# Kernel tuning notes

Hardware: AMD Instinct MI355X
Metric: run time of the kernel (lower is better)

## Reference

```python
import jax, jax.numpy as jnp
import numpy as np

N = 100000
E = 1600000
IN_C, HID_C, OUT_C = 40, 64, 3


def _sage_params(key, f_in, f_out):
    k1, k2, k3 = jax.random.split(key, 3)
    s = 1.0 / np.sqrt(f_in)
    return (jax.random.uniform(k1, (f_in, f_out), jnp.float32, -s, s),  # W_neigh (lin_l)
            jax.random.uniform(k2, (f_in, f_out), jnp.float32, -s, s),  # W_root  (lin_r)
            jax.random.uniform(k3, (f_out,), jnp.float32, -s, s))       # bias


def setup_inputs() -> dict:
    key = jax.random.key(0)
    ks = jax.random.split(key, 8)
    x = jax.random.normal(ks[0], (N, IN_C), jnp.float32)
    edge_index = jax.random.randint(ks[1], (2, E), 0, N, jnp.int64)
    dims = [(IN_C, HID_C), (HID_C, HID_C), (HID_C, OUT_C),   # encoder
            (OUT_C, HID_C), (HID_C, HID_C), (HID_C, IN_C)]   # decoder
    names = ['enc1', 'enc2', 'enc3', 'dec1', 'dec2', 'dec3']
    out = {'x': x, 'edge_index': edge_index}
    for name, (fi, fo), k in zip(names, dims, ks[2:]):
        Wl, Wr, b = _sage_params(k, fi, fo)
        out[name + '_Wl'] = Wl
        out[name + '_Wr'] = Wr
        out[name + '_b'] = b
    return out


def _sage_conv(h, src, dst, inv_deg, Wl, Wr, b):
    # mean-aggregate neighbor features (messages src -> dst), then linear.
    msg_sum = jax.ops.segment_sum(h[src], dst, num_segments=N)  # [N, F_in]
    agg = msg_sum * inv_deg                                      # mean aggregation
    return agg @ Wl + h @ Wr + b


def reference(x, edge_index,
              enc1_Wl, enc1_Wr, enc1_b, enc2_Wl, enc2_Wr, enc2_b,
              enc3_Wl, enc3_Wr, enc3_b, dec1_Wl, dec1_Wr, dec1_b,
              dec2_Wl, dec2_Wr, dec2_b, dec3_Wl, dec3_Wr, dec3_b):
    src, dst = edge_index[0], edge_index[1]
    deg = jax.ops.segment_sum(jnp.ones((E,), jnp.float32), dst, num_segments=N)
    inv_deg = (1.0 / jnp.maximum(deg, 1.0))[:, None]
    # encoder
    h = jax.nn.relu(_sage_conv(x, src, dst, inv_deg, enc1_Wl, enc1_Wr, enc1_b))
    h = jax.nn.relu(_sage_conv(h, src, dst, inv_deg, enc2_Wl, enc2_Wr, enc2_b))
    z = _sage_conv(h, src, dst, inv_deg, enc3_Wl, enc3_Wr, enc3_b)
    # decoder
    h = jax.nn.relu(_sage_conv(z, src, dst, inv_deg, dec1_Wl, dec1_Wr, dec1_b))
    h = jax.nn.relu(_sage_conv(h, src, dst, inv_deg, dec2_Wl, dec2_Wr, dec2_b))
    x_rec = _sage_conv(h, src, dst, inv_deg, dec3_Wl, dec3_Wr, dec3_b)
    return (x_rec, z)
```

## Files before the change

### kernel.cpp

```cpp
#include <hip/hip_runtime.h>
#include <stdint.h>

#define NNODES 100000
#define NEDGES 1600000
#define NB 98
#define WIN 25000
#define NSL 64
#define SLICE 25000

typedef unsigned short ushort_t;
typedef __attribute__((ext_vector_type(8))) short bf16x8;
typedef __attribute__((ext_vector_type(4))) float f32x4;

__device__ __forceinline__ float b2f(ushort_t u) {
  union { float f; uint32_t i; } v; v.i = ((uint32_t)u) << 16; return v.f;
}
__device__ __forceinline__ float blo(uint32_t p) {
  union { float f; uint32_t i; } v; v.i = p << 16; return v.f;
}
__device__ __forceinline__ float bhi(uint32_t p) {
  union { float f; uint32_t i; } v; v.i = p & 0xffff0000u; return v.f;
}
__device__ __forceinline__ ushort_t f2b(float f) {
  union { float f; uint32_t i; } v; v.f = f;
  uint32_t r = (v.i + 0x7fffu + ((v.i >> 16) & 1u)) >> 16;
  return (ushort_t)r;
}
__device__ __forceinline__ uint32_t pack2(float lo, float hi) {
  return (uint32_t)f2b(lo) | ((uint32_t)f2b(hi) << 16);
}
__device__ __forceinline__ int clampn(int i) {
  return i < 0 ? 0 : (i >= NNODES ? NNODES - 1 : i);
}

__global__ void detect_k(const uint32_t* __restrict__ x, const uint32_t* __restrict__ ei,
                         int* __restrict__ flags) {
  if (blockIdx.x == 0 && threadIdx.x == 0) {
    int cf = 0, ci = 0;
    for (int i = 0; i < 256; ++i) {
      uint32_t u = x[i];
      uint32_t e = (u >> 7) & 0xFFu;
      if (e >= 100u && e <= 141u) cf++;
      if (ei[2 * i + 1] == 0u) ci++;
    }
    flags[0] = (cf >= 128) ? 1 : 0;
    flags[1] = (ci >= 128) ? 1 : 0;
  }
}

__global__ void zero_i32(int* __restrict__ p, int n) {
  int i = blockIdx.x * blockDim.x + threadIdx.x;
  if (i < n) p[i] = 0;
}

__global__ __launch_bounds__(1024) void histw2_k(const uint32_t* __restrict__ ei,
                                                 int* __restrict__ degp,
                                                 const int* __restrict__ flags) {
  __shared__ int h[WIN];
  int b = blockIdx.x;
  int w = b >> 6, s = b & 63;
  for (int j = threadIdx.x; j < WIN; j += 1024) h[j] = 0;
  __syncthreads();
  int i64 = flags[1];
  int base = w * WIN;
  int e0 = s * SLICE, e1 = e0 + SLICE;
  for (int e = e0 + threadIdx.x; e < e1; e += 1024) {
    int d = i64 ? (int)ei[2 * (size_t)NEDGES + 2 * (size_t)e] : (int)ei[(size_t)NEDGES + e];
    d = clampn(d);
    int j = d - base;
    if ((unsigned)j < (unsigned)WIN) atomicAdd(&h[j], 1);
  }
  __syncthreads();
  int* dp = degp + (size_t)s * NNODES + base;
  for (int j = threadIdx.x; j < WIN; j += 1024) dp[j] = h[j];
}

__global__ void hreduce_k(int* __restrict__ degp, int* __restrict__ deg) {
  int n = blockIdx.x * blockDim.x + threadIdx.x;
  if (n >= NNODES) return;
  int run = 0;
  for (int s = 0; s < NSL; ++s) {
    size_t idx = (size_t)s * NNODES + n;
    int t = degp[idx];
    degp[idx] = run;
    run += t;
  }
  deg[n] = run;
}

__global__ __launch_bounds__(1024) void scan1_k(const int* __restrict__ deg, int* __restrict__ bsum) {
  __shared__ int wsum[16];
  int tid = threadIdx.x;
  int i = blockIdx.x * 1024 + tid;
  int v = (i < NNODES) ? deg[i] : 0;
  #pragma unroll
  for (int d = 32; d >= 1; d >>= 1) v += __shfl_down(v, d);
  if ((tid & 63) == 0) wsum[tid >> 6] = v;
  __syncthreads();
  if (tid == 0) {
    int t = 0;
    #pragma unroll
    for (int w = 0; w < 16; ++w) t += wsum[w];
    bsum[blockIdx.x] = t;
  }
}

__global__ void scan2_k(int* __restrict__ bsum, int* __restrict__ offs) {
  if (blockIdx.x == 0 && threadIdx.x == 0) {
    int run = 0;
    for (int b = 0; b < NB; ++b) { int t = bsum[b]; bsum[b] = run; run += t; }
    offs[NNODES] = run;
  }
}

__global__ __launch_bounds__(1024) void scan3_k(const int* __restrict__ deg, const int* __restrict__ bsum,
                                                int* __restrict__ offs, int* __restrict__ cursor,
                                                float* __restrict__ invd) {
  __shared__ int wsum[16];
  int tid = threadIdx.x;
  int lane = tid & 63, wid = tid >> 6;
  int i = blockIdx.x * 1024 + tid;
  int v = (i < NNODES) ? deg[i] : 0;
  int s = v;
  #pragma unroll
  for (int d = 1; d < 64; d <<= 1) {
    int t = __shfl_up(s, d);
    if (lane >= d) s += t;
  }
  if (lane == 63) wsum[wid] = s;
  __syncthreads();
  int wprefix = 0;
  #pragma unroll
  for (int w = 0; w < 16; ++w)
    if (w < wid) wprefix += wsum[w];
  if (i < NNODES) {
    int excl = bsum[blockIdx.x] + wprefix + s - v;
    offs[i] = excl;
    cursor[i] = excl;
    invd[i] = 1.0f / fmaxf((float)v, 1.0f);
  }
}

__global__ void scatter4_k(const uint32_t* __restrict__ ei, int* __restrict__ cursor,
                           int* __restrict__ csr, const int* __restrict__ flags,
                           int lo, int hi) {
  int e = blockIdx.x * blockDim.x + threadIdx.x;
  if (e >= NEDGES) return;
  int i64 = flags[1];
  int s, d;
  if (i64) {
    d = (int)ei[2 * (size_t)NEDGES + 2 * (size_t)e];
    d = clampn(d);
    if (d < lo || d >= hi) return;
    s = (int)ei[2 * (size_t)e];
  } else {
    d = (int)ei[(size_t)NEDGES + e];
    d = clampn(d);
    if (d < lo || d >= hi) return;
    s = (int)ei[e];
  }
  int p = atomicAdd(&cursor[d], 1);
  if (p >= 0 && p < NEDGES) csr[p] = clampn(s);
}

template <bool BF16>
__global__ void cvt_packx_k(const void* __restrict__ src, uint32_t* __restrict__ dst, int npairs,
                            const int* __restrict__ flags) {
  if (flags[0] != (BF16 ? 1 : 0)) return;
  int i = blockIdx.x * blockDim.x + threadIdx.x;
  if (i < npairs) {
    if constexpr (BF16) dst[i] = ((const uint32_t*)src)[i];
    else {
      const float* s = (const float*)src;
      dst[i] = pack2(s[2 * i], s[2 * i + 1]);
    }
  }
}

template <bool BF16>
__global__ void cvt_outp_k(const uint32_t* __restrict__ src, void* __restrict__ dst, int npairs,
                           const int* __restrict__ flags) {
  if (flags[0] != (BF16 ? 1 : 0)) return;
  int i = blockIdx.x * blockDim.x + threadIdx.x;
  if (i < npairs) {
    if constexpr (BF16) ((uint32_t*)dst)[i] = src[i];
    else {
      uint32_t w = src[i];
      float* d = (float*)dst;
      d[2 * i] = blo(w);
      d[2 * i + 1] = bhi(w);
    }
  }
}

template <bool BF16>
__global__ void cvt_out_k(const float* __restrict__ src, void* __restrict__ dst, int n,
                          const int* __restrict__ flags) {
  if (flags[0] != (BF16 ? 1 : 0)) return;
  int i = blockIdx.x * blockDim.x + threadIdx.x;
  if (i < n) {
    if constexpr (BF16) ((ushort_t*)dst)[i] = f2b(src[i]);
    else ((float*)dst)[i] = src[i];
  }
}

struct WPtrs { const void* p[18]; int sz[18]; int off[18]; };

template <bool BF16>
__global__ void cvt_w_k(WPtrs w, float* __restrict__ dst, const int* __restrict__ flags) {
  if (flags[0] != (BF16 ? 1 : 0)) return;
  int a = blockIdx.x;
  int sz = w.sz[a], off = w.off[a];
  for (int t = threadIdx.x; t < sz; t += blockDim.x) {
    dst[off + t] = BF16 ? b2f(((const ushort_t*)w.p[a])[t]) : ((const float*)w.p[a])[t];
  }
}

template <bool ADD_U>
__global__ __launch_bounds__(256) void agg3_k(const float* __restrict__ feat, const int* __restrict__ csr,
                                              const int* __restrict__ offs, const float* __restrict__ invd,
                                              const float* __restrict__ u, float* __restrict__ out) {
  int n = blockIdx.x * blockDim.x + threadIdx.x;
  if (n >= NNODES) return;
  int k0 = offs[n], k1 = offs[n + 1];
  float a0 = 0.f, a1 = 0.f, a2 = 0.f;
  int k = k0;
  for (; k + 4 <= k1; k += 4) {
    const float* r0 = feat + (size_t)clampn(csr[k]) * 3;
    const float* r1 = feat + (size_t)clampn(csr[k + 1]) * 3;
    const float* r2 = feat + (size_t)clampn(csr[k + 2]) * 3;
    const float* r3 = feat + (size_t)clampn(csr[k + 3]) * 3;
    a0 += r0[0] + r1[0] + r2[0] + r3[0];
    a1 += r0[1] + r1[1] + r2[1] + r3[1];
    a2 += r0[2] + r1[2] + r2[2] + r3[2];
  }
  for (; k < k1; ++k) {
    const float* r = feat + (size_t)clampn(csr[k]) * 3;
    a0 += r[0]; a1 += r[1]; a2 += r[2];
  }
  float iv = invd[n];
  a0 *= iv; a1 *= iv; a2 *= iv;
  if constexpr (ADD_U) {
    a0 += u[(size_t)n * 3];
    a1 += u[(size_t)n * 3 + 1];
    a2 += u[(size_t)n * 3 + 2];
  }
  out[(size_t)n * 3]     = a0;
  out[(size_t)n * 3 + 1] = a1;
  out[(size_t)n * 3 + 2] = a2;
}

template <int PAIRS, bool ADD_U>
__global__ __launch_bounds__(256) void aggp4_k(const uint32_t* __restrict__ feat, const int* __restrict__ csr,
                                               const int* __restrict__ offs, const float* __restrict__ invd,
                                               const uint32_t* __restrict__ u, uint32_t* __restrict__ out) {
  constexpr int HP = PAIRS / 2;
  int lane = threadIdx.x & 63;
  int n = (blockIdx.x * blockDim.x + threadIdx.x) >> 6;
  if (n >= NNODES) return;
  int q = lane >> 4;
  int p = lane & 15;
  int k0 = offs[n], k1 = offs[n + 1];
  float a0 = 0.f, a1 = 0.f, a2 = 0.f, a3 = 0.f;
  int k = k0;
  for (; k + 8 <= k1; k += 8) {
    int r0 = clampn(csr[k + q]);
    int r1 = clampn(csr[k + 4 + q]);
    if (p < HP) {
      uint2 w0 = ((const uint2*)(feat + (size_t)r0 * PAIRS))[p];
      uint2 w1 = ((const uint2*)(feat + (size_t)r1 * PAIRS))[p];
      a0 += blo(w0.x) + blo(w1.x);
      a1 += bhi(w0.x) + bhi(w1.x);
      a2 += blo(w0.y) + blo(w1.y);
      a3 += bhi(w0.y) + bhi(w1.y);
    }
  }
  for (; k + 4 <= k1; k += 4) {
    int r0 = clampn(csr[k + q]);
    if (p < HP) {
      uint2 w0 = ((const uint2*)(feat + (size_t)r0 * PAIRS))[p];
      a0 += blo(w0.x); a1 += bhi(w0.x); a2 += blo(w0.y); a3 += bhi(w0.y);
    }
  }
  int rem = k1 - k;
  if (q < rem && p < HP) {
    int r0 = clampn(csr[k + q]);
    uint2 w0 = ((const uint2*)(feat + (size_t)r0 * PAIRS))[p];
    a0 += blo(w0.x); a1 += bhi(w0.x); a2 += blo(w0.y); a3 += bhi(w0.y);
  }
  a0 += __shfl_xor(a0, 16); a0 += __shfl_xor(a0, 32);
  a1 += __shfl_xor(a1, 16); a1 += __shfl_xor(a1, 32);
  a2 += __shfl_xor(a2, 16); a2 += __shfl_xor(a2, 32);
  a3 += __shfl_xor(a3, 16); a3 += __shfl_xor(a3, 32);
  if (q == 0 && p < HP) {
    float iv = invd[n];
    float v0 = a0 * iv, v1 = a1 * iv, v2 = a2 * iv, v3 = a3 * iv;
    if constexpr (ADD_U) {
      uint2 uw = ((const uint2*)(u + (size_t)n * PAIRS))[p];
      v0 += blo(uw.x); v1 += bhi(uw.x); v2 += blo(uw.y); v3 += bhi(uw.y);
    }
    uint2 ow;
    ow.x = pack2(v0, v1);
    ow.y = pack2(v2, v3);
    ((uint2*)(out + (size_t)n * PAIRS))[p] = ow;
  }
}

template <int F_IN, int F_OUT, bool DUAL, bool RELU, bool PIN, bool POUT>
__global__ __launch_bounds__(256) void mgemm_k(const void* __restrict__ Av, const void* __restrict__ Bv,
                                               const float* __restrict__ W1, const float* __restrict__ W2,
                                               const float* __restrict__ Wb,
                                               void* __restrict__ C1v, void* __restrict__ C2v) {
  constexpr int KS = (F_IN + 31) / 32;
  constexpr int JT = (F_OUT + 15) / 16;
  constexpr int PP = F_IN / 2;
  int lane = threadIdx.x & 63;
  int wid  = threadIdx.x >> 6;
  int tile = blockIdx.x * 4 + wid;
  if (tile * 16 >= NNODES) return;
  int l15 = lane & 15, l4 = lane >> 4;

  bf16x8 w1f[KS][JT], w2f[KS][JT];
  float bv[JT];
  #pragma unroll
  for (int ks = 0; ks < KS; ++ks) {
    #pragma unroll
    for (int jt = 0; jt < JT; ++jt) {
      int col = jt * 16 + l15;
      #pragma unroll
      for (int j = 0; j < 8; ++j) {
        int k = ks * 32 + l4 * 8 + j;
        bool ok = (k < F_IN) && (col < F_OUT);
        w1f[ks][jt][j] = ok ? (short)f2b(W1[k * F_OUT + col]) : (short)0;
        w2f[ks][jt][j] = ok ? (short)f2b(W2[k * F_OUT + col]) : (short)0;
      }
    }
  }
  #pragma unroll
  for (int jt = 0; jt < JT; ++jt) {
    int col = jt * 16 + l15;
    bv[jt] = (col < F_OUT) ? Wb[col] : 0.f;
  }

  int row = tile * 16 + l15;
  bf16x8 af[KS], bfr[KS];
  if constexpr (PIN) {
    const uint32_t* Arow = (const uint32_t*)Av + (size_t)row * PP;
    #pragma unroll
    for (int ks = 0; ks < KS; ++ks) {
      #pragma unroll
      for (int w4 = 0; w4 < 4; ++w4) {
        int word = ks * 16 + l4 * 4 + w4;
        uint32_t v = (word < PP) ? Arow[word] : 0u;
        af[ks][2 * w4]     = (short)(v & 0xffffu);
        af[ks][2 * w4 + 1] = (short)(v >> 16);
      }
    }
    if constexpr (!DUAL) {
      const uint32_t* Brow = (const uint32_t*)Bv + (size_t)row * PP;
      #pragma unroll
      for (int ks = 0; ks < KS; ++ks) {
        #pragma unroll
        for (int w4 = 0; w4 < 4; ++w4) {
          int word = ks * 16 + l4 * 4 + w4;
          uint32_t v = (word < PP) ? Brow[word] : 0u;
          bfr[ks][2 * w4]     = (short)(v & 0xffffu);
          bfr[ks][2 * w4 + 1] = (short)(v >> 16);
        }
      }
    }
  } else {
    const float* Arow = (const float*)Av + (size_t)row * F_IN;
    #pragma unroll
    for (int ks = 0; ks < KS; ++ks) {
      #pragma unroll
      for (int j = 0; j < 8; ++j) {
        int k = ks * 32 + l4 * 8 + j;
        af[ks][j] = (k < F_IN) ? (short)f2b(Arow[k]) : (short)0;
      }
    }
    if constexpr (!DUAL) {
      const float* Brow = (const float*)Bv + (size_t)row * F_IN;
      #pragma unroll
      for (int ks = 0; ks < KS; ++ks) {
        #pragma unroll
        for (int j = 0; j < 8; ++j) {
          int k = ks * 32 + l4 * 8 + j;
          bfr[ks][j] = (k < F_IN) ? (short)f2b(Brow[k]) : (short)0;
        }
      }
    }
  }

  f32x4 acc1[JT], acc2[DUAL ? JT : 1];
  #pragma unroll
  for (int jt = 0; jt < JT; ++jt) {
    acc1[jt] = (f32x4)(0.f);
    if constexpr (DUAL) acc2[jt] = (f32x4)(0.f);
  }

  #pragma unroll
  for (int ks = 0; ks < KS; ++ks) {
    #pragma unroll
    for (int jt = 0; jt < JT; ++jt) {
      acc1[jt] = __builtin_amdgcn_mfma_f32_16x16x32_bf16(af[ks], w1f[ks][jt], acc1[jt], 0, 0, 0);
      if constexpr (DUAL)
        acc2[jt] = __builtin_amdgcn_mfma_f32_16x16x32_bf16(af[ks], w2f[ks][jt], acc2[jt], 0, 0, 0);
      else
        acc1[jt] = __builtin_amdgcn_mfma_f32_16x16x32_bf16(bfr[ks], w2f[ks][jt], acc1[jt], 0, 0, 0);
    }
  }

  #pragma unroll
  for (int jt = 0; jt < JT; ++jt) {
    int col = jt * 16 + l15;
    #pragma unroll
    for (int r = 0; r < 4; ++r) {
      int orow = tile * 16 + l4 * 4 + r;
      if constexpr (DUAL) {
        float v1 = acc1[jt][r];
        float v2 = acc2[jt][r] + bv[jt];
        if constexpr (POUT) {
          float p1 = __shfl_xor(v1, 1);
          float p2 = __shfl_xor(v2, 1);
          if (((lane & 1) == 0) && col < F_OUT) {
            ((uint32_t*)C1v)[(size_t)orow * (F_OUT / 2) + (col >> 1)] = pack2(v1, p1);
            ((uint32_t*)C2v)[(size_t)orow * (F_OUT / 2) + (col >> 1)] = pack2(v2, p2);
          }
        } else {
          if (col < F_OUT) {
            ((float*)C1v)[(size_t)orow * F_OUT + col] = v1;
            ((float*)C2v)[(size_t)orow * F_OUT + col] = v2;
          }
        }
      } else {
        float v = acc1[jt][r] + bv[jt];
        if constexpr (RELU) v = fmaxf(v, 0.f);
        if constexpr (POUT) {
          float pv = __shfl_xor(v, 1);
          if (((lane & 1) == 0) && col < F_OUT)
            ((uint32_t*)C1v)[(size_t)orow * (F_OUT / 2) + (col >> 1)] = pack2(v, pv);
        } else {
          if (col < F_OUT)
            ((float*)C1v)[(size_t)orow * F_OUT + col] = v;
        }
      }
    }
  }
}

extern "C" void kernel_launch(void* const* d_in, const int* in_sizes, int n_in,
                              void* d_out, int out_size, void* d_ws, size_t ws_size,
                              hipStream_t stream) {
  const uint32_t* xw = (const uint32_t*)d_in[0];
  const uint32_t* ei = (const uint32_t*)d_in[1];

  char* ws = (char*)d_ws;
  size_t off = 0;
  auto carve = [&](size_t bytes) -> char* {
    char* p = ws + off;
    off = (off + bytes + 255) & ~(size_t)255;
    return p;
  };
  int* flags     = (int*)carve(8);
  int* deg       = (int*)carve((size_t)NNODES * 4);
  int* offs      = (int*)carve((size_t)(NNODES + 1) * 4);
  int* cursor    = (int*)carve((size_t)NNODES * 4);
  float* invd    = (float*)carve((size_t)NNODES * 4);
  int* bsum      = (int*)carve((size_t)NB * 4);
  int* csr       = (int*)carve((size_t)NEDGES * 4);
  float* wf      = (float*)carve((size_t)32768 * 4);
  uint32_t* xp   = (uint32_t*)carve((size_t)NNODES * 20 * 4);
  uint32_t* mp   = (uint32_t*)carve((size_t)NNODES * 20 * 4);
  uint32_t* b0p  = (uint32_t*)carve((size_t)NNODES * 32 * 4);
  uint32_t* b1p  = (uint32_t*)carve((size_t)NNODES * 32 * 4);
  uint32_t* b2p  = (uint32_t*)carve((size_t)NNODES * 32 * 4);
  uint32_t* y40p = (uint32_t*)carve((size_t)NNODES * 20 * 4);
  uint32_t* u40p = (uint32_t*)carve((size_t)NNODES * 20 * 4);
  uint32_t* xrp  = (uint32_t*)carve((size_t)NNODES * 20 * 4);
  float* y3f     = (float*)carve((size_t)NNODES * 3 * 4);
  float* u3f     = (float*)carve((size_t)NNODES * 3 * 4);
  float* zf      = (float*)carve((size_t)NNODES * 3 * 4);
  float* m3f     = (float*)carve((size_t)NNODES * 3 * 4);

  int* degp = (int*)b0p;

  static const int wsz[18] = {2560, 2560, 64, 4096, 4096, 64, 192, 192, 3,
                              192, 192, 64, 4096, 4096, 64, 2560, 2560, 40};
  WPtrs wp;
  int woff = 0;
  for (int i = 0; i < 18; ++i) {
    wp.p[i] = d_in[2 + i];
    wp.sz[i] = wsz[i];
    wp.off[i] = woff;
    woff += wsz[i];
  }
  const float* W[18];
  for (int i = 0; i < 18; ++i) W[i] = wf + wp.off[i];

  detect_k<<<1, 64, 0, stream>>>(xw, ei, flags);
  zero_i32<<<(NEDGES + 255) / 256, 256, 0, stream>>>(csr, NEDGES);
  histw2_k<<<4 * NSL, 1024, 0, stream>>>(ei, degp, flags);
  hreduce_k<<<(NNODES + 255) / 256, 256, 0, stream>>>(degp, deg);
  scan1_k<<<NB, 1024, 0, stream>>>(deg, bsum);
  scan2_k<<<1, 64, 0, stream>>>(bsum, offs);
  scan3_k<<<NB, 1024, 0, stream>>>(deg, bsum, offs, cursor, invd);
  const int EB = (NEDGES + 255) / 256;
  scatter4_k<<<EB, 256, 0, stream>>>(ei, cursor, csr, flags, 0, 25000);
  scatter4_k<<<EB, 256, 0, stream>>>(ei, cursor, csr, flags, 25000, 50000);
  scatter4_k<<<EB, 256, 0, stream>>>(ei, cursor, csr, flags, 50000, 75000);
  scatter4_k<<<EB, 256, 0, stream>>>(ei, cursor, csr, flags, 75000, 100000);

  const int NXP = NNODES * 20;
  cvt_packx_k<false><<<(NXP + 255) / 256, 256, 0, stream>>>(d_in[0], xp, NXP, flags);
  cvt_packx_k<true ><<<(NXP + 255) / 256, 256, 0, stream>>>(d_in[0], xp, NXP, flags);
  cvt_w_k<false><<<18, 256, 0, stream>>>(wp, wf, flags);
  cvt_w_k<true ><<<18, 256, 0, stream>>>(wp, wf, flags);

  const int AGGW_BLOCKS = (NNODES * 64 + 255) / 256;
  const int AGG3_BLOCKS = (NNODES + 255) / 256;
  const int MG = (NNODES / 16 + 3) / 4;

  aggp4_k<20, false><<<AGGW_BLOCKS, 256, 0, stream>>>(xp, csr, offs, invd, nullptr, mp);
  mgemm_k<40, 64, false, true, true, true><<<MG, 256, 0, stream>>>(mp, xp, W[0], W[1], W[2], b1p, nullptr);
  aggp4_k<32, false><<<AGGW_BLOCKS, 256, 0, stream>>>(b1p, csr, offs, invd, nullptr, b0p);
  mgemm_k<64, 64, false, true, true, true><<<MG, 256, 0, stream>>>(b0p, b1p, W[3], W[4], W[5], b2p, nullptr);
  mgemm_k<64, 3, true, false, true, false><<<MG, 256, 0, stream>>>(b2p, nullptr, W[6], W[7], W[8], y3f, u3f);
  agg3_k<true><<<AGG3_BLOCKS, 256, 0, stream>>>(y3f, csr, offs, invd, u3f, zf);
  agg3_k<false><<<AGG3_BLOCKS, 256, 0, stream>>>(zf, csr, offs, invd, nullptr, m3f);
  mgemm_k<3, 64, false, true, false, true><<<MG, 256, 0, stream>>>(m3f, zf, W[9], W[10], W[11], b1p, nullptr);
  aggp4_k<32, false><<<AGGW_BLOCKS, 256, 0, stream>>>(b1p, csr, offs, invd, nullptr, b0p);
  mgemm_k<64, 64, false, true, true, true><<<MG, 256, 0, stream>>>(b0p, b1p, W[12], W[13], W[14], b2p, nullptr);
  mgemm_k<64, 40, true, false, true, true><<<MG, 256, 0, stream>>>(b2p, nullptr, W[15], W[16], W[17], y40p, u40p);
  aggp4_k<20, true><<<AGGW_BLOCKS, 256, 0, stream>>>(y40p, csr, offs, invd, u40p, xrp);

  const int NX = NNODES * 40;
  const int NZ = NNODES * 3;
  cvt_outp_k<false><<<(NXP + 255) / 256, 256, 0, stream>>>(xrp, d_out, NXP, flags);
  cvt_outp_k<true ><<<(NXP + 255) / 256, 256, 0, stream>>>(xrp, d_out, NXP, flags);
  cvt_out_k<false><<<(NZ + 255) / 256, 256, 0, stream>>>(zf, (float*)d_out + NX, NZ, flags);
  cvt_out_k<true ><<<(NZ + 255) / 256, 256, 0, stream>>>(zf, (ushort_t*)d_out + NX, NZ, flags);
  (void)in_sizes; (void)n_in; (void)out_size; (void)ws_size;
}
```

Measured before the change: 504.5 us.

## Split 64-wide aggregation into XCD-mapped column halves for L2 locality

```diff
diff --git a/kernel.cpp b/kernel.cpp
--- a/kernel.cpp
+++ b/kernel.cpp
@@ -303,6 +303,54 @@
     ow.x = pack2(v0, v1);
     ow.y = pack2(v2, v3);
     ((uint2*)(out + (size_t)n * PAIRS))[p] = ow;
+  }
+}
+
+template <bool ADD_U>
+__global__ __launch_bounds__(256) void aggph_k(const uint32_t* __restrict__ feat, const int* __restrict__ csr,
+                                               const int* __restrict__ offs, const float* __restrict__ invd,
+                                               const uint32_t* __restrict__ u, uint32_t* __restrict__ out) {
+  constexpr int PAIRS = 32;
+  int b = blockIdx.x;
+  int xcd = b & 7;
+  int half = xcd >> 2;
+  int hb = (xcd & 3) * 6250 + (b >> 3);
+  int wid = threadIdx.x >> 6;
+  int lane = threadIdx.x & 63;
+  int n = hb * 4 + wid;
+  if (n >= NNODES) return;
+  int o = lane >> 3;
+  int p = lane & 7;
+  const uint32_t* tbl = feat + half * 16;
+  int k0 = offs[n], k1 = offs[n + 1];
+  float a0 = 0.f, a1 = 0.f, a2 = 0.f, a3 = 0.f;
+  int k = k0;
+  for (; k + 8 <= k1; k += 8) {
+    int r = clampn(csr[k + o]);
+    uint2 w = ((const uint2*)(tbl + (size_t)r * PAIRS))[p];
+    a0 += blo(w.x); a1 += bhi(w.x); a2 += blo(w.y); a3 += bhi(w.y);
+  }
+  int rem = k1 - k;
+  if (o < rem) {
+    int r = clampn(csr[k + o]);
+    uint2 w = ((const uint2*)(tbl + (size_t)r * PAIRS))[p];
+    a0 += blo(w.x); a1 += bhi(w.x); a2 += blo(w.y); a3 += bhi(w.y);
+  }
+  a0 += __shfl_xor(a0, 8); a0 += __shfl_xor(a0, 16); a0 += __shfl_xor(a0, 32);
+  a1 += __shfl_xor(a1, 8); a1 += __shfl_xor(a1, 16); a1 += __shfl_xor(a1, 32);
+  a2 += __shfl_xor(a2, 8); a2 += __shfl_xor(a2, 16); a2 += __shfl_xor(a2, 32);
+  a3 += __shfl_xor(a3, 8); a3 += __shfl_xor(a3, 16); a3 += __shfl_xor(a3, 32);
+  if (o == 0) {
+    float iv = invd[n];
+    float v0 = a0 * iv, v1 = a1 * iv, v2 = a2 * iv, v3 = a3 * iv;
+    if constexpr (ADD_U) {
+      uint2 uw = ((const uint2*)(u + (size_t)n * PAIRS + half * 16))[p];
+      v0 += blo(uw.x); v1 += bhi(uw.x); v2 += blo(uw.y); v3 += bhi(uw.y);
+    }
+    uint2 ow;
+    ow.x = pack2(v0, v1);
+    ow.y = pack2(v2, v3);
+    ((uint2*)(out + (size_t)n * PAIRS + half * 16))[p] = ow;
   }
 }
 
@@ -518,18 +566,19 @@
   cvt_w_k<true ><<<18, 256, 0, stream>>>(wp, wf, flags);
 
   const int AGGW_BLOCKS = (NNODES * 64 + 255) / 256;
+  const int AGGH_BLOCKS = 50000;
   const int AGG3_BLOCKS = (NNODES + 255) / 256;
   const int MG = (NNODES / 16 + 3) / 4;
 
   aggp4_k<20, false><<<AGGW_BLOCKS, 256, 0, stream>>>(xp, csr, offs, invd, nullptr, mp);
   mgemm_k<40, 64, false, true, true, true><<<MG, 256, 0, stream>>>(mp, xp, W[0], W[1], W[2], b1p, nullptr);
-  aggp4_k<32, false><<<AGGW_BLOCKS, 256, 0, stream>>>(b1p, csr, offs, invd, nullptr, b0p);
+  aggph_k<false><<<AGGH_BLOCKS, 256, 0, stream>>>(b1p, csr, offs, invd, nullptr, b0p);
   mgemm_k<64, 64, false, true, true, true><<<MG, 256, 0, stream>>>(b0p, b1p, W[3], W[4], W[5], b2p, nullptr);
   mgemm_k<64, 3, true, false, true, false><<<MG, 256, 0, stream>>>(b2p, nullptr, W[6], W[7], W[8], y3f, u3f);
   agg3_k<true><<<AGG3_BLOCKS, 256, 0, stream>>>(y3f, csr, offs, invd, u3f, zf);
   agg3_k<false><<<AGG3_BLOCKS, 256, 0, stream>>>(zf, csr, offs, invd, nullptr, m3f);
   mgemm_k<3, 64, false, true, false, true><<<MG, 256, 0, stream>>>(m3f, zf, W[9], W[10], W[11], b1p, nullptr);
-  aggp4_k<32, false><<<AGGW_BLOCKS, 256, 0, stream>>>(b1p, csr, offs, invd, nullptr, b0p);
+  aggph_k<false><<<AGGH_BLOCKS, 256, 0, stream>>>(b1p, csr, offs, invd, nullptr, b0p);
   mgemm_k<64, 64, false, true, true, true><<<MG, 256, 0, stream>>>(b0p, b1p, W[12], W[13], W[14], b2p, nullptr);
   mgemm_k<64, 40, true, false, true, true><<<MG, 256, 0, stream>>>(b2p, nullptr, W[15], W[16], W[17], y40p, u40p);
   aggp4_k<20, true><<<AGGW_BLOCKS, 256, 0, stream>>>(y40p, csr, offs, invd, u40p, xrp);
```

Result: slower. 570.3 us (+13.0%).
